# Performance work log

Hardware: AMD Instinct MI355X
Metric: run time of the kernel (lower is better)

## Reference

```python
import jax, jax.numpy as jnp
import numpy as np

B, L, D, N = 8, 1024, 1024, 32  # N = d_state // 2 (complex conjugate-pair modes)
DT_MIN, DT_MAX = 0.001, 0.1


def setup_inputs() -> dict:
    key = jax.random.key(0)
    ks = jax.random.split(key, 12)
    s = 1.0 / np.sqrt(D)  # torch Linear / Conv1d default init bound
    inp = {
        "x": jax.random.normal(ks[0], (B, L, D), jnp.float32),
        "in_W": jax.random.uniform(ks[1], (D, D), jnp.float32, -s, s),
        "in_b": jax.random.uniform(ks[2], (D,), jnp.float32, -s, s),
        # S4D kernel params
        "log_dt": (np.log(DT_MIN)
                   + jax.random.uniform(ks[3], (D,), jnp.float32)
                   * (np.log(DT_MAX) - np.log(DT_MIN))).astype(jnp.float32),
        "C": jax.random.normal(ks[4], (D, N, 2), jnp.float32),  # complex C as (re, im)
        "log_A_real": jnp.log(0.5 * jnp.ones((D, N), jnp.float32)),
        "A_imag": jnp.tile((np.pi * jnp.arange(N, dtype=np.float32))[None, :], (D, 1)),
        "D_skip": jax.random.normal(ks[5], (D,), jnp.float32),
        # output_linear = Conv1d(D, 2D, 1) + GLU(dim=-2); kernel squeezed to (2D, D)
        "glu_W": jax.random.uniform(ks[6], (2 * D, D), jnp.float32, -s, s),
        "glu_b": jax.random.uniform(ks[7], (2 * D,), jnp.float32, -s, s),
        "out_W": jax.random.uniform(ks[8], (D, D), jnp.float32, -s, s),
        "out_b": jax.random.uniform(ks[9], (D,), jnp.float32, -s, s),
    }
    return inp


def reference(x, in_W, in_b, log_dt, C, log_A_real, A_imag, D_skip,
              glu_W, glu_b, out_W, out_b):
    # in_proj
    x_in = x @ in_W.T + in_b                      # (B, L, D)
    u = jnp.swapaxes(x_in, 1, 2)                  # (B, D, L) -- transposed=False path
    Lseq = u.shape[-1]

    # ---- S4D kernel (ZOH-like discretization of diagonal SSM) ----
    dt = jnp.exp(log_dt)                          # (D,)
    Cc = (C[..., 0] + 1j * C[..., 1]).astype(jnp.complex64)   # (D, N)
    A = (-jnp.exp(log_A_real) + 1j * A_imag).astype(jnp.complex64)
    dtA = A * dt[:, None].astype(jnp.complex64)   # (D, N)
    # Vandermonde: exp(dtA * l) for l in [0, L)
    K = jnp.exp(dtA[:, :, None] * jnp.arange(Lseq, dtype=jnp.float32))  # (D, N, L)
    Ceff = Cc * (jnp.exp(dtA) - 1.0) / A
    k = 2.0 * jnp.einsum('hn,hnl->hl', Ceff, K).real            # (D, L)

    # ---- FFT causal convolution ----
    n = 2 * Lseq
    k_f = jnp.fft.rfft(k, n=n)                    # (D, L+1)
    u_f = jnp.fft.rfft(u, n=n)                    # (B, D, L+1)
    y = jnp.fft.irfft(u_f * k_f, n=n)[..., :Lseq] # (B, D, L)

    y = y + u * D_skip[:, None]                   # skip connection
    y = jax.nn.gelu(y, approximate=False)         # torch nn.GELU (erf)

    # Conv1d(D, 2D, kernel=1) + GLU over channel dim
    z = jnp.einsum('oh,bhl->bol', glu_W, y) + glu_b[None, :, None]
    a, g = jnp.split(z, 2, axis=1)
    y = a * jax.nn.sigmoid(g)                     # (B, D, L)

    y = jnp.swapaxes(y, 1, 2)                     # (B, L, D)
    out = y @ out_W.T + out_b
    return out + x
```

## Files before the change

kernel.cpp:

```cpp
#include <hip/hip_runtime.h>
#include <math.h>

#define BB 8
#define LL 1024
#define DD 1024
#define KD 1024
#define NM 32
#define NCH 16
#define CL 64
#define NTOK (BB * LL)

typedef __bf16 bf16_t;
typedef __bf16 bf16x8 __attribute__((ext_vector_type(8)));
typedef __bf16 bf16x4 __attribute__((ext_vector_type(4)));
typedef float  f32x4  __attribute__((ext_vector_type(4)));

__device__ __forceinline__ float gelu_f(float z)
{
    float t = fmaf(0.044715f * z * z, z, z);
    return z / (1.f + expf(-1.5957691216f * t));
}

__global__ __launch_bounds__(256)
void f2b_all_kernel(const float* __restrict__ x,    bf16_t* __restrict__ xb,
                    const float* __restrict__ w0,   bf16_t* __restrict__ d0,
                    const float* __restrict__ w1,   bf16_t* __restrict__ d1,
                    const float* __restrict__ w2,   bf16_t* __restrict__ d2)
{
    int b = blockIdx.x;
    const float* s; bf16_t* d; int base;
    if (b < 8192)       { s = x;  d = xb; base = b; }
    else if (b < 9216)  { s = w0; d = d0; base = b - 8192; }
    else if (b < 11264) { s = w1; d = d1; base = b - 9216; }
    else                { s = w2; d = d2; base = b - 11264; }
    int i = (base * 256 + threadIdx.x) * 4;
    float4 f = *(const float4*)(s + i);
    bf16x4 o = { (bf16_t)f.x, (bf16_t)f.y, (bf16_t)f.z, (bf16_t)f.w };
    *(bf16x4*)(d + i) = o;
}

__device__ __forceinline__ void stage128x32(const bf16_t* __restrict__ g,
                                            bf16_t* lds, int tid)
{
    #pragma unroll
    for (int q = 0; q < 2; ++q) {
        const bf16_t* src = g + (size_t)(q * 64 + (tid >> 2)) * KD + (tid & 3) * 8;
        bf16_t* dst = lds + q * 2048 + tid * 8;
        __builtin_amdgcn_global_load_lds(
            (const __attribute__((address_space(1))) void*)src,
            (__attribute__((address_space(3))) void*)dst, 16, 0, 0);
    }
}

template<int MODE>
__global__ __launch_bounds__(256)
void gemm_bk64_kernel(const bf16_t* __restrict__ A, const bf16_t* __restrict__ B,
                      const float* __restrict__ bias, const float* __restrict__ res,
                      void* __restrict__ outp, int ldo)
{
    __shared__ bf16_t As[2][128 * 32];
    __shared__ bf16_t Bs[2][128 * 32];
    const int tid = threadIdx.x;
    const int lane = tid & 63, w = tid >> 6;
    const int wy = w >> 1, wx = w & 1;
    const int m0 = blockIdx.y << 7, n0 = blockIdx.x << 7;
    const bf16_t* Ag = A + (size_t)m0 * KD;
    const bf16_t* Bg = B + (size_t)n0 * KD;
    f32x4 acc[4][4] = {};
    const int lm = lane & 15;
    const int ks = (lane >> 4) << 3;

    for (int k0 = 0; k0 < KD; k0 += 64) {
        stage128x32(Ag + k0,      As[0], tid);
        stage128x32(Bg + k0,      Bs[0], tid);
        stage128x32(Ag + k0 + 32, As[1], tid);
        stage128x32(Bg + k0 + 32, Bs[1], tid);
        __syncthreads();
        #pragma unroll
        for (int p = 0; p < 2; ++p) {
            bf16x8 af[4], bfr[4];
            #pragma unroll
            for (int i = 0; i < 4; ++i)
                af[i] = *(bf16x8*)&As[p][((wy << 6) + (i << 4) + lm) * 32 + ks];
            #pragma unroll
            for (int j = 0; j < 4; ++j)
                bfr[j] = *(bf16x8*)&Bs[p][((wx << 6) + (j << 4) + lm) * 32 + ks];
            #pragma unroll
            for (int i = 0; i < 4; ++i)
                #pragma unroll
                for (int j = 0; j < 4; ++j)
                    acc[i][j] = __builtin_amdgcn_mfma_f32_16x16x32_bf16(
                                    af[i], bfr[j], acc[i][j], 0, 0, 0);
        }
        __syncthreads();
    }

    const int row4 = (lane >> 4) << 2;
    #pragma unroll
    for (int i = 0; i < 4; ++i) {
        #pragma unroll
        for (int r = 0; r < 4; ++r) {
            int m = m0 + (wy << 6) + (i << 4) + row4 + r;
            #pragma unroll
            for (int j = 0; j < 4; ++j) {
                int n = n0 + (wx << 6) + (j << 4) + lm;
                float v = acc[i][j][r];
                if (MODE == 0) {
                    ((bf16_t*)outp)[(size_t)m * ldo + n] = (bf16_t)(v + bias[m]);
                } else if (MODE == 1) {
                    ((bf16_t*)outp)[(size_t)m * ldo + n] = (bf16_t)(v + bias[n]);
                } else {
                    ((float*)outp)[(size_t)m * ldo + n] =
                        v + bias[n] + res[(size_t)m * ldo + n];
                }
            }
        }
    }
}

__global__ __launch_bounds__(256)
void glu_combine_kernel(const bf16_t* __restrict__ z, bf16_t* __restrict__ v)
{
    int i = blockIdx.x * 256 + threadIdx.x;
    int m = i >> 7, n8 = (i & 127) << 3;
    const bf16_t* zp = z + (size_t)m * 2048 + n8;
    bf16x8 za = *(const bf16x8*)zp;
    bf16x8 zg = *(const bf16x8*)(zp + 1024);
    bf16x8 o;
    #pragma unroll
    for (int e = 0; e < 8; ++e) {
        float a = (float)za[e], gg = (float)zg[e];
        o[e] = (bf16_t)(a / (1.f + expf(-gg)));
    }
    *(bf16x8*)(v + (size_t)m * 1024 + n8) = o;
}

__global__ __launch_bounds__(64)
void genVTP_kernel(const float* __restrict__ log_dt, const float* __restrict__ lar,
                   const float* __restrict__ aim, const float* __restrict__ Cp,
                   const float* __restrict__ dskip,
                   bf16_t* __restrict__ V, bf16_t* __restrict__ TP)
{
    const int tid = threadIdx.x;
    if (blockIdx.x < DD / 2) {
        const int h = blockIdx.x * 2 + (tid >> 5);
        const int n = tid & 31;
        const float dt = expf(log_dt[h]);
        const float ardt = -expf(lar[h * NM + n]) * dt;
        const float aidt = aim[h * NM + n] * dt;
        float sn, cs;
        sincosf(aidt, &sn, &cs);
        float er = expf(ardt);
        float wr = er * cs, wi = er * sn;
        float inv = 1.f / fmaf(wr, wr, wi * wi);
        float vr = wr * inv, vi = -wi * inv;
        sincosf(63.f * aidt, &sn, &cs);
        er = expf(63.f * ardt);
        float pr = er * cs, pi = er * sn;
        bf16_t* rowr = V + ((size_t)h * 64 + 2 * n) * 64;
        bf16_t* rowi = rowr + 64;
        #pragma unroll
        for (int c8 = 0; c8 < 8; ++c8) {
            bf16x8 rr, ri;
            #pragma unroll
            for (int e = 0; e < 8; ++e) {
                rr[e] = (bf16_t)pr; ri[e] = (bf16_t)pi;
                float t = fmaf(pr, vr, -pi * vi);
                pi = fmaf(pr, vi, pi * vr);
                pr = t;
            }
            *(bf16x8*)(rowr + c8 * 8) = rr;
            *(bf16x8*)(rowi + c8 * 8) = ri;
        }
        return;
    }
    __shared__ float ardt_s[NM], aidt_s[NM], cr_s[NM], ci_s[NM], K_s[CL];
    const int h = blockIdx.x - DD / 2;
    const float dt = expf(log_dt[h]);
    if (tid < NM) {
        int n = tid;
        float ar = -expf(lar[h * NM + n]);
        float ai = aim[h * NM + n];
        float sn, cs;
        sincosf(ai * dt, &sn, &cs);
        float er = expf(ar * dt);
        float wrr = er * cs, wii = er * sn;
        float Crr = Cp[(h * NM + n) * 2 + 0];
        float Cii = Cp[(h * NM + n) * 2 + 1];
        float nr = fmaf(Crr, wrr - 1.f, -Cii * wii);
        float ni = fmaf(Crr, wii, Cii * (wrr - 1.f));
        float inv = 2.f / fmaf(ar, ar, ai * ai);
        cr_s[n] = fmaf(nr, ar, ni * ai) * inv;
        ci_s[n] = fmaf(ni, ar, -nr * ai) * inv;
        ardt_s[n] = ar * dt;
        aidt_s[n] = ai * dt;
    }
    __syncthreads();
    {
        float d = (float)tid;
        float kv = (tid == 0) ? dskip[h] : 0.f;
        #pragma unroll 8
        for (int n = 0; n < NM; ++n) {
            float sn, cs;
            sincosf(aidt_s[n] * d, &sn, &cs);
            float e = expf(ardt_s[n] * d);
            kv = fmaf(cr_s[n], e * cs, kv);
            kv = fmaf(-ci_s[n], e * sn, kv);
        }
        K_s[tid] = kv;
    }
    __syncthreads();
    const int i = tid;
    bf16_t* row = TP + ((size_t)h * CL + i) * 128;
    #pragma unroll
    for (int c8 = 0; c8 < 8; ++c8) {
        bf16x8 v;
        #pragma unroll
        for (int e = 0; e < 8; ++e) {
            int l = c8 * 8 + e;
            v[e] = (l <= i) ? (bf16_t)K_s[i - l] : (bf16_t)0.f;
        }
        *(bf16x8*)(row + c8 * 8) = v;
    }
    const float fi = (float)(i + 1);
    #pragma unroll
    for (int c8 = 0; c8 < 8; ++c8) {
        bf16x8 v;
        #pragma unroll
        for (int q = 0; q < 4; ++q) {
            int n = c8 * 4 + q;
            float sn, cs;
            sincosf(aidt_s[n] * fi, &sn, &cs);
            float e = expf(ardt_s[n] * fi);
            float Wr = e * cs, Wi = e * sn;
            v[2 * q]     = (bf16_t)(fmaf(cr_s[n], Wr, -ci_s[n] * Wi));
            v[2 * q + 1] = (bf16_t)(-fmaf(cr_s[n], Wi, ci_s[n] * Wr));
        }
        *(bf16x8*)(row + 64 + c8 * 8) = v;
    }
}

__global__ __launch_bounds__(256)
void ssm_fused_kernel(const bf16_t* __restrict__ u_ch, const bf16_t* __restrict__ V,
                      const bf16_t* __restrict__ TP,
                      const float* __restrict__ log_dt, const float* __restrict__ lar,
                      const float* __restrict__ aim, bf16_t* __restrict__ y_bi)
{
    __shared__ float  Sbc_s[128 * 64];
    __shared__ bf16_t Sc_s[128 * 64];
    const int h = blockIdx.x;
    const int tid = threadIdx.x;
    const int lane = tid & 63, w = tid >> 6;
    const int lm = lane & 15, ks = (lane >> 4) << 3;
    const bf16_t* U   = u_ch + (size_t)h * 8192;
    const bf16_t* Vh  = V    + (size_t)h * 4096;
    const bf16_t* TPh = TP   + (size_t)h * 8192;

    bf16x8 af_u[2][2];
    #pragma unroll
    for (int im = 0; im < 2; ++im)
        #pragma unroll
        for (int kk = 0; kk < 2; ++kk)
            af_u[im][kk] = *(const bf16x8*)(U + (((w << 1) + im) * 16 + lm) * 64
                                            + kk * 32 + ks);

    f32x4 acc1[2][4] = {};
    #pragma unroll
    for (int kk = 0; kk < 2; ++kk) {
        bf16x8 bfr[4];
        #pragma unroll
        for (int jn = 0; jn < 4; ++jn)
            bfr[jn] = *(const bf16x8*)(Vh + (jn * 16 + lm) * 64 + kk * 32 + ks);
        #pragma unroll
        for (int im = 0; im < 2; ++im)
            #pragma unroll
            for (int jn = 0; jn < 4; ++jn)
                acc1[im][jn] = __builtin_amdgcn_mfma_f32_16x16x32_bf16(
                                   af_u[im][kk], bfr[jn], acc1[im][jn], 0, 0, 0);
    }
    const int r4 = (lane >> 4) << 2;
    #pragma unroll
    for (int im = 0; im < 2; ++im)
        #pragma unroll
        for (int jn = 0; jn < 4; ++jn)
            #pragma unroll
            for (int r = 0; r < 4; ++r)
                Sbc_s[(((w << 1) + im) * 16 + r4 + r) * 64 + jn * 16 + lm]
                    = acc1[im][jn][r];
    __syncthreads();

    {
        const int b = tid >> 5, n = tid & 31;
        const float dtv = expf(log_dt[h]);
        const float ardt = -expf(lar[h * NM + n]) * dtv;
        const float aidt = aim[h * NM + n] * dtv;
        float sn, cs;
        sincosf(64.f * aidt, &sn, &cs);
        float er = expf(64.f * ardt);
        const float gr = er * cs, gi = er * sn;
        float sr = 0.f, si = 0.f;
        for (int c = 0; c < NCH; ++c) {
            int idx = (b * 16 + c) * 64 + 2 * n;
            float lr = Sbc_s[idx], li = Sbc_s[idx + 1];
            Sc_s[idx]     = (bf16_t)sr;
            Sc_s[idx + 1] = (bf16_t)si;
            float t0 = fmaf(gr, sr, fmaf(-gi, si, lr));
            si = fmaf(gr, si, fmaf(gi, sr, li));
            sr = t0;
        }
    }
    __syncthreads();

    f32x4 acc2[2][4] = {};
    #pragma unroll
    for (int kk = 0; kk < 4; ++kk) {
        bf16x8 af[2], bfr[4];
        #pragma unroll
        for (int im = 0; im < 2; ++im) {
            if (kk < 2)
                af[im] = af_u[im][kk];
            else
                af[im] = *(bf16x8*)&Sc_s[(((w << 1) + im) * 16 + lm) * 64
                                         + (kk - 2) * 32 + ks];
        }
        #pragma unroll
        for (int jn = 0; jn < 4; ++jn)
            bfr[jn] = *(const bf16x8*)(TPh + (jn * 16 + lm) * 128 + kk * 32 + ks);
        #pragma unroll
        for (int im = 0; im < 2; ++im)
            #pragma unroll
            for (int jn = 0; jn < 4; ++jn)
                acc2[im][jn] = __builtin_amdgcn_mfma_f32_16x16x32_bf16(
                                   af[im], bfr[jn], acc2[im][jn], 0, 0, 0);
    }
    bf16_t* out = y_bi + (size_t)h * 8192;
    #pragma unroll
    for (int im = 0; im < 2; ++im)
        #pragma unroll
        for (int jn = 0; jn < 4; ++jn)
            #pragma unroll
            for (int r = 0; r < 4; ++r) {
                int batch = ((w << 1) + im) * 16 + r4 + r;
                int i = jn * 16 + lm;
                out[batch * 64 + i] = (bf16_t)gelu_f(acc2[im][jn][r]);
            }
}

__global__ __launch_bounds__(256)
void transpose_kernel(const bf16_t* __restrict__ src, bf16_t* __restrict__ dst,
                      int src_rows, int src_cols)
{
    __shared__ unsigned short tile[64][68];
    const int tid = threadIdx.x;
    const int c0 = blockIdx.x << 6, r0 = blockIdx.y << 6;
    const int r = tid >> 4, c4 = (tid & 15) << 2;
    #pragma unroll
    for (int p = 0; p < 4; ++p) {
        int rr = p * 16 + r;
        ushort4 v = *(const ushort4*)((const unsigned short*)src +
                                      (size_t)(r0 + rr) * src_cols + c0 + c4);
        *(ushort4*)&tile[rr][c4] = v;
    }
    __syncthreads();
    #pragma unroll
    for (int p = 0; p < 4; ++p) {
        int rr = p * 16 + r;
        ushort4 v;
        v.x = tile[c4 + 0][rr];
        v.y = tile[c4 + 1][rr];
        v.z = tile[c4 + 2][rr];
        v.w = tile[c4 + 3][rr];
        *(ushort4*)((unsigned short*)dst + (size_t)(c0 + rr) * src_rows + r0 + c4) = v;
    }
}

extern "C" void kernel_launch(void* const* d_in, const int* in_sizes, int n_in,
                              void* d_out, int out_size, void* d_ws, size_t ws_size,
                              hipStream_t stream)
{
    (void)in_sizes; (void)n_in; (void)out_size; (void)ws_size;
    const float* x      = (const float*)d_in[0];
    const float* in_W   = (const float*)d_in[1];
    const float* in_b   = (const float*)d_in[2];
    const float* log_dt = (const float*)d_in[3];
    const float* Cp     = (const float*)d_in[4];
    const float* lar    = (const float*)d_in[5];
    const float* aim    = (const float*)d_in[6];
    const float* dsk    = (const float*)d_in[7];
    const float* gluW   = (const float*)d_in[8];
    const float* glub   = (const float*)d_in[9];
    const float* outW   = (const float*)d_in[10];
    const float* outb   = (const float*)d_in[11];

    char* ws = (char*)d_ws;
    bf16_t* xb    = (bf16_t*)(ws);
    bf16_t* TP    = (bf16_t*)(ws);
    bf16_t* y_tok = (bf16_t*)(ws);
    bf16_t* vb    = (bf16_t*)(ws);
    bf16_t* V     = (bf16_t*)(ws + 16777216);
    bf16_t* z     = (bf16_t*)(ws + 16777216);
    bf16_t* u_ch  = (bf16_t*)(ws + 33554432);
    bf16_t* wbin  = (bf16_t*)(ws + 50331648);
    bf16_t* wbglu = (bf16_t*)(ws + 52428800);
    bf16_t* wbout = (bf16_t*)(ws + 56623104);
    bf16_t* y_bi  = (bf16_t*)d_out;

    f2b_all_kernel<<<dim3(12288), dim3(256), 0, stream>>>(
        x, xb, in_W, wbin, gluW, wbglu, outW, wbout);

    gemm_bk64_kernel<0><<<dim3(NTOK / 128, DD / 128), dim3(256), 0, stream>>>(
        wbin, xb, in_b, nullptr, u_ch, NTOK);

    genVTP_kernel<<<dim3(DD / 2 + DD), dim3(64), 0, stream>>>(
        log_dt, lar, aim, Cp, dsk, V, TP);
    ssm_fused_kernel<<<dim3(DD), dim3(256), 0, stream>>>(
        u_ch, V, TP, log_dt, lar, aim, y_bi);

    transpose_kernel<<<dim3(NTOK / 64, DD / 64), dim3(256), 0, stream>>>(y_bi, y_tok, DD, NTOK);
    gemm_bk64_kernel<1><<<dim3(2048 / 128, NTOK / 128), dim3(256), 0, stream>>>(
        y_tok, wbglu, glub, nullptr, z, 2048);
    glu_combine_kernel<<<dim3(NTOK * DD / 8 / 256), dim3(256), 0, stream>>>(z, vb);
    gemm_bk64_kernel<2><<<dim3(DD / 128, NTOK / 128), dim3(256), 0, stream>>>(
        vb, wbout, outb, x, d_out, DD);
}
```

Measured before the change: 289.5 us.

## Rewrite GEMMs as triple-buffered 256x128 tiles with swizzled LDS and fused GLU

Replaces the 128x128 GEMM kernel with a 512-thread 256x128-tile kernel. It triple-buffers K tiles of 64 in dynamic LDS and issues loads two tiles ahead, using explicit waitcnt and barriers to overlap global loads with MFMA. It adds an XOR swizzle on LDS columns to avoid bank conflicts, remaps block IDs across XCDs, and fuses the GLU gate into the GLU GEMM by accumulating both halves in one block, which removes the z intermediate and the separate combine kernel. The cost is higher register pressure from the dual accumulators and 144KB of LDS per block, which limits occupancy.

```diff
diff --git a/kernel.cpp b/kernel.cpp
--- a/kernel.cpp
+++ b/kernel.cpp
@@ -9,6 +9,7 @@
 #define NCH 16
 #define CL 64
 #define NTOK (BB * LL)
+#define GSMEM 147456
 
 typedef __bf16 bf16_t;
 typedef __bf16 bf16x8 __attribute__((ext_vector_type(8)));
@@ -39,100 +40,138 @@
     *(bf16x4*)(d + i) = o;
 }
 
-__device__ __forceinline__ void stage128x32(const bf16_t* __restrict__ g,
-                                            bf16_t* lds, int tid)
-{
-    #pragma unroll
-    for (int q = 0; q < 2; ++q) {
-        const bf16_t* src = g + (size_t)(q * 64 + (tid >> 2)) * KD + (tid & 3) * 8;
-        bf16_t* dst = lds + q * 2048 + tid * 8;
+__device__ __forceinline__ void stage_tile(const bf16_t* __restrict__ Ag,
+                                           const bf16_t* __restrict__ Bg,
+                                           bf16_t* Asb, bf16_t* Bsb, int tid)
+{
+    #pragma unroll
+    for (int p = 0; p < 4; ++p) {
+        int e = p * 512 + tid;
+        int row = e >> 3, c8 = (e & 7) << 3;
+        int sc = c8 ^ ((row & 7) << 3);
         __builtin_amdgcn_global_load_lds(
-            (const __attribute__((address_space(1))) void*)src,
-            (__attribute__((address_space(3))) void*)dst, 16, 0, 0);
+            (const __attribute__((address_space(1))) void*)(Ag + (size_t)row * KD + sc),
+            (__attribute__((address_space(3))) void*)(Asb + e * 8), 16, 0, 0);
+    }
+    #pragma unroll
+    for (int p = 0; p < 2; ++p) {
+        int e = p * 512 + tid;
+        int row = e >> 3, c8 = (e & 7) << 3;
+        int sc = c8 ^ ((row & 7) << 3);
+        __builtin_amdgcn_global_load_lds(
+            (const __attribute__((address_space(1))) void*)(Bg + (size_t)row * KD + sc),
+            (__attribute__((address_space(3))) void*)(Bsb + e * 8), 16, 0, 0);
+    }
+}
+
+__device__ __forceinline__ void compute_tile(const bf16_t* Asb, const bf16_t* Bsb,
+                                             int wy, int wx, int lm, int ks,
+                                             f32x4 (&acc)[4][4])
+{
+    #pragma unroll
+    for (int kk = 0; kk < 2; ++kk) {
+        bf16x8 af[4], bfr[4];
+        const int col = kk * 32 + ks;
+        #pragma unroll
+        for (int i = 0; i < 4; ++i) {
+            int row = wy * 64 + i * 16 + lm;
+            af[i] = *(const bf16x8*)(Asb + row * 64 + (col ^ ((row & 7) << 3)));
+        }
+        #pragma unroll
+        for (int j = 0; j < 4; ++j) {
+            int row = wx * 64 + j * 16 + lm;
+            bfr[j] = *(const bf16x8*)(Bsb + row * 64 + (col ^ ((row & 7) << 3)));
+        }
+        __builtin_amdgcn_s_setprio(1);
+        #pragma unroll
+        for (int i = 0; i < 4; ++i)
+            #pragma unroll
+            for (int j = 0; j < 4; ++j)
+                acc[i][j] = __builtin_amdgcn_mfma_f32_16x16x32_bf16(
+                                af[i], bfr[j], acc[i][j], 0, 0, 0);
+        __builtin_amdgcn_s_setprio(0);
     }
 }
 
 template<int MODE>
-__global__ __launch_bounds__(256)
-void gemm_bk64_kernel(const bf16_t* __restrict__ A, const bf16_t* __restrict__ B,
-                      const float* __restrict__ bias, const float* __restrict__ res,
-                      void* __restrict__ outp, int ldo)
-{
-    __shared__ bf16_t As[2][128 * 32];
-    __shared__ bf16_t Bs[2][128 * 32];
+__global__ __launch_bounds__(512, 2)
+void gemm3_kernel(const bf16_t* __restrict__ A, const bf16_t* __restrict__ B,
+                  const float* __restrict__ bias, const float* __restrict__ res,
+                  void* __restrict__ outp)
+{
+    extern __shared__ __align__(16) bf16_t lds[];
+    bf16_t* As0 = lds;
+    bf16_t* Bs0 = lds + 3 * 16384;
+
     const int tid = threadIdx.x;
     const int lane = tid & 63, w = tid >> 6;
     const int wy = w >> 1, wx = w & 1;
-    const int m0 = blockIdx.y << 7, n0 = blockIdx.x << 7;
-    const bf16_t* Ag = A + (size_t)m0 * KD;
-    const bf16_t* Bg = B + (size_t)n0 * KD;
-    f32x4 acc[4][4] = {};
-    const int lm = lane & 15;
-    const int ks = (lane >> 4) << 3;
-
-    for (int k0 = 0; k0 < KD; k0 += 64) {
-        stage128x32(Ag + k0,      As[0], tid);
-        stage128x32(Bg + k0,      Bs[0], tid);
-        stage128x32(Ag + k0 + 32, As[1], tid);
-        stage128x32(Bg + k0 + 32, Bs[1], tid);
-        __syncthreads();
-        #pragma unroll
-        for (int p = 0; p < 2; ++p) {
-            bf16x8 af[4], bfr[4];
-            #pragma unroll
-            for (int i = 0; i < 4; ++i)
-                af[i] = *(bf16x8*)&As[p][((wy << 6) + (i << 4) + lm) * 32 + ks];
-            #pragma unroll
-            for (int j = 0; j < 4; ++j)
-                bfr[j] = *(bf16x8*)&Bs[p][((wx << 6) + (j << 4) + lm) * 32 + ks];
-            #pragma unroll
-            for (int i = 0; i < 4; ++i)
-                #pragma unroll
-                for (int j = 0; j < 4; ++j)
-                    acc[i][j] = __builtin_amdgcn_mfma_f32_16x16x32_bf16(
-                                    af[i], bfr[j], acc[i][j], 0, 0, 0);
-        }
-        __syncthreads();
-    }
-
-    const int row4 = (lane >> 4) << 2;
-    #pragma unroll
-    for (int i = 0; i < 4; ++i) {
+    const int lm = lane & 15, ks = (lane >> 4) << 3;
+
+    const int nbx = gridDim.x;
+    int bid = blockIdx.y * nbx + blockIdx.x;
+    const int cpx = (gridDim.x * gridDim.y) >> 3;
+    bid = (bid & 7) * cpx + (bid >> 3);
+    const int by = bid / nbx, bx = bid % nbx;
+    const int m0 = by * 256, n0 = bx * 128;
+
+    const bf16_t* Ag     = A + (size_t)m0 * KD;
+    const bf16_t* Bbase0 = B + (size_t)n0 * KD;
+    const bf16_t* Bbase1 = (MODE == 1) ? B + (size_t)(1024 + n0) * KD : Bbase0;
+    const int NTT = (MODE == 1) ? 32 : 16;
+
+    f32x4 acc[4][4]  = {};
+    f32x4 acc2[4][4] = {};
+
+    stage_tile(Ag,      Bbase0,      As0,         Bs0,        tid);
+    stage_tile(Ag + 64, Bbase0 + 64, As0 + 16384, Bs0 + 8192, tid);
+    asm volatile("s_waitcnt vmcnt(6)" ::: "memory");
+    __builtin_amdgcn_s_barrier();
+
+    #pragma unroll 1
+    for (int t = 0; t < NTT; ++t) {
+        if (t + 2 < NTT) {
+            int q2 = (t + 2) % 3;
+            const bf16_t* Agt = Ag + ((t + 2) & 15) * 64;
+            const bf16_t* Bgt = ((MODE == 1 && t + 2 >= 16) ? Bbase1 : Bbase0)
+                                + ((t + 2) & 15) * 64;
+            stage_tile(Agt, Bgt, As0 + q2 * 16384, Bs0 + q2 * 8192, tid);
+        }
+        int q = t % 3;
+        if (MODE == 1 && t >= 16)
+            compute_tile(As0 + q * 16384, Bs0 + q * 8192, wy, wx, lm, ks, acc2);
+        else
+            compute_tile(As0 + q * 16384, Bs0 + q * 8192, wy, wx, lm, ks, acc);
+        if (t + 1 < NTT) {
+            if (t + 2 < NTT) asm volatile("s_waitcnt vmcnt(6) lgkmcnt(0)" ::: "memory");
+            else             asm volatile("s_waitcnt vmcnt(0) lgkmcnt(0)" ::: "memory");
+            __builtin_amdgcn_s_barrier();
+        }
+    }
+
+    const int r4 = (lane >> 4) << 2;
+    #pragma unroll
+    for (int i = 0; i < 4; ++i)
         #pragma unroll
         for (int r = 0; r < 4; ++r) {
-            int m = m0 + (wy << 6) + (i << 4) + row4 + r;
+            int m = m0 + wy * 64 + i * 16 + r4 + r;
             #pragma unroll
             for (int j = 0; j < 4; ++j) {
-                int n = n0 + (wx << 6) + (j << 4) + lm;
-                float v = acc[i][j][r];
+                int n = n0 + wx * 64 + j * 16 + lm;
                 if (MODE == 0) {
-                    ((bf16_t*)outp)[(size_t)m * ldo + n] = (bf16_t)(v + bias[m]);
+                    ((bf16_t*)outp)[(size_t)m * 8192 + n] =
+                        (bf16_t)(acc[i][j][r] + bias[m]);
                 } else if (MODE == 1) {
-                    ((bf16_t*)outp)[(size_t)m * ldo + n] = (bf16_t)(v + bias[n]);
+                    float a = acc[i][j][r]  + bias[n];
+                    float g = acc2[i][j][r] + bias[1024 + n];
+                    ((bf16_t*)outp)[(size_t)m * 1024 + n] =
+                        (bf16_t)(a / (1.f + expf(-g)));
                 } else {
-                    ((float*)outp)[(size_t)m * ldo + n] =
-                        v + bias[n] + res[(size_t)m * ldo + n];
+                    ((float*)outp)[(size_t)m * 1024 + n] =
+                        acc[i][j][r] + bias[n] + res[(size_t)m * 1024 + n];
                 }
             }
         }
-    }
-}
-
-__global__ __launch_bounds__(256)
-void glu_combine_kernel(const bf16_t* __restrict__ z, bf16_t* __restrict__ v)
-{
-    int i = blockIdx.x * 256 + threadIdx.x;
-    int m = i >> 7, n8 = (i & 127) << 3;
-    const bf16_t* zp = z + (size_t)m * 2048 + n8;
-    bf16x8 za = *(const bf16x8*)zp;
-    bf16x8 zg = *(const bf16x8*)(zp + 1024);
-    bf16x8 o;
-    #pragma unroll
-    for (int e = 0; e < 8; ++e) {
-        float a = (float)za[e], gg = (float)zg[e];
-        o[e] = (bf16_t)(a / (1.f + expf(-gg)));
-    }
-    *(bf16x8*)(v + (size_t)m * 1024 + n8) = o;
 }
 
 __global__ __launch_bounds__(64)
@@ -396,20 +435,30 @@
     bf16_t* xb    = (bf16_t*)(ws);
     bf16_t* TP    = (bf16_t*)(ws);
     bf16_t* y_tok = (bf16_t*)(ws);
-    bf16_t* vb    = (bf16_t*)(ws);
     bf16_t* V     = (bf16_t*)(ws + 16777216);
-    bf16_t* z     = (bf16_t*)(ws + 16777216);
+    bf16_t* vb    = (bf16_t*)(ws + 16777216);
     bf16_t* u_ch  = (bf16_t*)(ws + 33554432);
     bf16_t* wbin  = (bf16_t*)(ws + 50331648);
     bf16_t* wbglu = (bf16_t*)(ws + 52428800);
     bf16_t* wbout = (bf16_t*)(ws + 56623104);
     bf16_t* y_bi  = (bf16_t*)d_out;
 
+    static bool s_attr = false;
+    if (!s_attr) {
+        hipFuncSetAttribute((const void*)gemm3_kernel<0>,
+                            hipFuncAttributeMaxDynamicSharedMemorySize, GSMEM);
+        hipFuncSetAttribute((const void*)gemm3_kernel<1>,
+                            hipFuncAttributeMaxDynamicSharedMemorySize, GSMEM);
+        hipFuncSetAttribute((const void*)gemm3_kernel<2>,
+                            hipFuncAttributeMaxDynamicSharedMemorySize, GSMEM);
+        s_attr = true;
+    }
+
     f2b_all_kernel<<<dim3(12288), dim3(256), 0, stream>>>(
         x, xb, in_W, wbin, gluW, wbglu, outW, wbout);
 
-    gemm_bk64_kernel<0><<<dim3(NTOK / 128, DD / 128), dim3(256), 0, stream>>>(
-        wbin, xb, in_b, nullptr, u_ch, NTOK);
+    gemm3_kernel<0><<<dim3(NTOK / 128, DD / 256), dim3(512), GSMEM, stream>>>(
+        wbin, xb, in_b, nullptr, u_ch);
 
     genVTP_kernel<<<dim3(DD / 2 + DD), dim3(64), 0, stream>>>(
         log_dt, lar, aim, Cp, dsk, V, TP);
@@ -417,9 +466,9 @@
         u_ch, V, TP, log_dt, lar, aim, y_bi);
 
     transpose_kernel<<<dim3(NTOK / 64, DD / 64), dim3(256), 0, stream>>>(y_bi, y_tok, DD, NTOK);
-    gemm_bk64_kernel<1><<<dim3(2048 / 128, NTOK / 128), dim3(256), 0, stream>>>(
-        y_tok, wbglu, glub, nullptr, z, 2048);
-    glu_combine_kernel<<<dim3(NTOK * DD / 8 / 256), dim3(256), 0, stream>>>(z, vb);
-    gemm_bk64_kernel<2><<<dim3(DD / 128, NTOK / 128), dim3(256), 0, stream>>>(
-        vb, wbout, outb, x, d_out, DD);
-}
+    gemm3_kernel<1><<<dim3(1024 / 128, NTOK / 256), dim3(512), GSMEM, stream>>>(
+        y_tok, wbglu, glub, nullptr, vb);
+
+    gemm3_kernel<2><<<dim3(DD / 128, NTOK / 256), dim3(512), GSMEM, stream>>>(
+        vb, wbout, outb, x, d_out);
+}
```

After: 293.0 us. About the same (+1.2%).

## Double-buffer GEMM K-tiles with XOR-swizzled LDS layout

Applied to the files above, without the earlier changes.

Rewrites the bf16 MFMA GEMM so the global-to-LDS load of the next 64-wide K tile is issued before computing on the current one, using two LDS buffers and one barrier per iteration instead of two. The LDS tile is stored as 64-wide rows with an XOR swizzle on the 16-byte column chunk to reduce bank conflicts on the fragment reads. This doubles LDS use to 64 KB per block and adds a launch_bounds hint of two blocks per CU, which may limit occupancy. There is also a hazard risk: with no wait on the asynchronous loads before the barrier, the compiler's vmcnt handling has to be relied on for correctness.

```diff
diff --git a/kernel.cpp b/kernel.cpp
--- a/kernel.cpp
+++ b/kernel.cpp
@@ -39,27 +39,36 @@
     *(bf16x4*)(d + i) = o;
 }
 
-__device__ __forceinline__ void stage128x32(const bf16_t* __restrict__ g,
-                                            bf16_t* lds, int tid)
-{
-    #pragma unroll
-    for (int q = 0; q < 2; ++q) {
-        const bf16_t* src = g + (size_t)(q * 64 + (tid >> 2)) * KD + (tid & 3) * 8;
-        bf16_t* dst = lds + q * 2048 + tid * 8;
-        __builtin_amdgcn_global_load_lds(
-            (const __attribute__((address_space(1))) void*)src,
-            (__attribute__((address_space(3))) void*)dst, 16, 0, 0);
+#define GLL(gp, lp) __builtin_amdgcn_global_load_lds( \
+    (const __attribute__((address_space(1))) void*)(gp), \
+    (__attribute__((address_space(3))) void*)(lp), 16, 0, 0)
+
+__device__ __forceinline__ void stage_tile(const bf16_t* __restrict__ Ag,
+                                           const bf16_t* __restrict__ Bg,
+                                           bf16_t* Asb, bf16_t* Bsb, int tid)
+{
+    #pragma unroll
+    for (int p = 0; p < 4; ++p) {
+        int e = p * 256 + tid;
+        int row = e >> 3, sc = ((e & 7) ^ (row & 7)) << 3;
+        GLL(Ag + (size_t)row * KD + sc, Asb + e * 8);
+    }
+    #pragma unroll
+    for (int p = 0; p < 4; ++p) {
+        int e = p * 256 + tid;
+        int row = e >> 3, sc = ((e & 7) ^ (row & 7)) << 3;
+        GLL(Bg + (size_t)row * KD + sc, Bsb + e * 8);
     }
 }
 
 template<int MODE>
-__global__ __launch_bounds__(256)
-void gemm_bk64_kernel(const bf16_t* __restrict__ A, const bf16_t* __restrict__ B,
-                      const float* __restrict__ bias, const float* __restrict__ res,
-                      void* __restrict__ outp, int ldo)
-{
-    __shared__ bf16_t As[2][128 * 32];
-    __shared__ bf16_t Bs[2][128 * 32];
+__global__ __launch_bounds__(256, 2)
+void gemm_db_kernel(const bf16_t* __restrict__ A, const bf16_t* __restrict__ B,
+                    const float* __restrict__ bias, const float* __restrict__ res,
+                    void* __restrict__ outp, int ldo)
+{
+    __shared__ bf16_t As[2][128 * 64];
+    __shared__ bf16_t Bs[2][128 * 64];
     const int tid = threadIdx.x;
     const int lane = tid & 63, w = tid >> 6;
     const int wy = w >> 1, wx = w & 1;
@@ -68,23 +77,31 @@
     const bf16_t* Bg = B + (size_t)n0 * KD;
     f32x4 acc[4][4] = {};
     const int lm = lane & 15;
-    const int ks = (lane >> 4) << 3;
-
-    for (int k0 = 0; k0 < KD; k0 += 64) {
-        stage128x32(Ag + k0,      As[0], tid);
-        stage128x32(Bg + k0,      Bs[0], tid);
-        stage128x32(Ag + k0 + 32, As[1], tid);
-        stage128x32(Bg + k0 + 32, Bs[1], tid);
-        __syncthreads();
-        #pragma unroll
-        for (int p = 0; p < 2; ++p) {
+    const int qq = lane >> 4;
+
+    stage_tile(Ag, Bg, As[0], Bs[0], tid);
+    __syncthreads();
+
+    int buf = 0;
+    #pragma unroll 1
+    for (int t = 0; t < 16; ++t) {
+        if (t + 1 < 16)
+            stage_tile(Ag + (t + 1) * 64, Bg + (t + 1) * 64,
+                       As[buf ^ 1], Bs[buf ^ 1], tid);
+        #pragma unroll
+        for (int kk = 0; kk < 2; ++kk) {
             bf16x8 af[4], bfr[4];
-            #pragma unroll
-            for (int i = 0; i < 4; ++i)
-                af[i] = *(bf16x8*)&As[p][((wy << 6) + (i << 4) + lm) * 32 + ks];
-            #pragma unroll
-            for (int j = 0; j < 4; ++j)
-                bfr[j] = *(bf16x8*)&Bs[p][((wx << 6) + (j << 4) + lm) * 32 + ks];
+            const int g = (kk << 2) + qq;
+            #pragma unroll
+            for (int i = 0; i < 4; ++i) {
+                int row = (wy << 6) + (i << 4) + lm;
+                af[i] = *(const bf16x8*)&As[buf][row * 64 + ((g ^ (row & 7)) << 3)];
+            }
+            #pragma unroll
+            for (int j = 0; j < 4; ++j) {
+                int row = (wx << 6) + (j << 4) + lm;
+                bfr[j] = *(const bf16x8*)&Bs[buf][row * 64 + ((g ^ (row & 7)) << 3)];
+            }
             #pragma unroll
             for (int i = 0; i < 4; ++i)
                 #pragma unroll
@@ -93,6 +110,7 @@
                                     af[i], bfr[j], acc[i][j], 0, 0, 0);
         }
         __syncthreads();
+        buf ^= 1;
     }
 
     const int row4 = (lane >> 4) << 2;
@@ -408,7 +426,7 @@
     f2b_all_kernel<<<dim3(12288), dim3(256), 0, stream>>>(
         x, xb, in_W, wbin, gluW, wbglu, outW, wbout);
 
-    gemm_bk64_kernel<0><<<dim3(NTOK / 128, DD / 128), dim3(256), 0, stream>>>(
+    gemm_db_kernel<0><<<dim3(NTOK / 128, DD / 128), dim3(256), 0, stream>>>(
         wbin, xb, in_b, nullptr, u_ch, NTOK);
 
     genVTP_kernel<<<dim3(DD / 2 + DD), dim3(64), 0, stream>>>(
@@ -417,9 +435,9 @@
         u_ch, V, TP, log_dt, lar, aim, y_bi);
 
     transpose_kernel<<<dim3(NTOK / 64, DD / 64), dim3(256), 0, stream>>>(y_bi, y_tok, DD, NTOK);
-    gemm_bk64_kernel<1><<<dim3(2048 / 128, NTOK / 128), dim3(256), 0, stream>>>(
+    gemm_db_kernel<1><<<dim3(2048 / 128, NTOK / 128), dim3(256), 0, stream>>>(
         y_tok, wbglu, glub, nullptr, z, 2048);
     glu_combine_kernel<<<dim3(NTOK * DD / 8 / 256), dim3(256), 0, stream>>>(z, vb);
-    gemm_bk64_kernel<2><<<dim3(DD / 128, NTOK / 128), dim3(256), 0, stream>>>(
+    gemm_db_kernel<2><<<dim3(DD / 128, NTOK / 128), dim3(256), 0, stream>>>(
         vb, wbout, outb, x, d_out, DD);
 }
```

Measured after the change: 290.8 us. About the same (+0.4%).
